# Optimization experiments

Hardware: AMD Instinct MI355X
Metric: run time of the kernel (lower is better)

Reference implementation:

```python
import jax, jax.numpy as jnp
import numpy as np

D = 128
N = 20000
E = 640000
EPS = 1e-5


def setup_inputs() -> dict:
    key = jax.random.key(0)
    ks = jax.random.split(key, 12)
    x = jax.random.normal(ks[0], (N, D), dtype=jnp.float32)
    edge_index = jax.random.randint(ks[1], (2, E), 0, N, dtype=jnp.int64)
    edge_weight = jax.random.uniform(ks[2], (E,), dtype=jnp.float32)
    s = 1.0 / np.sqrt(D)
    # GraphConv params: lin_rel (bias=True) applied to aggregated messages,
    # lin_root (bias=False) applied to root features.
    W_rel = jax.random.uniform(ks[3], (D, D), minval=-s, maxval=s, dtype=jnp.float32)
    b_rel = jax.random.uniform(ks[4], (D,), minval=-s, maxval=s, dtype=jnp.float32)
    W_root = jax.random.uniform(ks[5], (D, D), minval=-s, maxval=s, dtype=jnp.float32)
    # add_linear Linear(out, out)
    lin_W = jax.random.uniform(ks[6], (D, D), minval=-s, maxval=s, dtype=jnp.float32)
    lin_b = jax.random.uniform(ks[7], (D,), minval=-s, maxval=s, dtype=jnp.float32)
    # LayerNorm affine params
    gamma = jnp.ones((D,), dtype=jnp.float32)
    beta = jnp.zeros((D,), dtype=jnp.float32)
    return {"x": x, "edge_index": edge_index, "edge_weight": edge_weight,
            "W_rel": W_rel, "b_rel": b_rel, "W_root": W_root,
            "lin_W": lin_W, "lin_b": lin_b, "gamma": gamma, "beta": beta}


def _layer_norm(h, gamma, beta):
    mu = jnp.mean(h, axis=-1, keepdims=True)
    var = jnp.mean(jnp.square(h - mu), axis=-1, keepdims=True)
    return (h - mu) * jax.lax.rsqrt(var + EPS) * gamma + beta


def reference(x, edge_index, edge_weight, W_rel, b_rel, W_root, lin_W, lin_b, gamma, beta):
    n = x.shape[0]
    src, dst = edge_index[0], edge_index[1]
    # message: edge_weight * x_j, gathered from source nodes
    msg = x[src] * edge_weight[:, None]                      # [E, D]
    # max aggregation to destination nodes; empty segments -> 0 (PyG fill)
    agg = jax.ops.segment_max(msg, dst, num_segments=n)      # [N, D]
    agg = jnp.where(jnp.isneginf(agg), 0.0, agg)
    # GraphConv: lin_rel(agg) + lin_root(x)
    h = agg @ W_rel.T + b_rel + x @ W_root.T                  # [N, D]
    # act + skip + norm
    h = jax.nn.gelu(h, approximate=False) + x
    h = _layer_norm(h, gamma, beta)
    # add_linear branch: act(lin(h)) + skip, then norm (module reuses self.norm)
    h2 = jax.nn.gelu(h @ lin_W.T + lin_b, approximate=False) + h
    h2 = _layer_norm(h2, gamma, beta)
    return h2, edge_weight
```

## Files before the change

### kernel.cpp

```cpp
#include <hip/hip_runtime.h>
#include <math.h>

#define N_NODES 20000
#define N_DIM   128
#define N_EDGES 640000
#define LN_EPS  1e-5f
#define NPW 4
#define CAP 80

#define TASK_E (N_EDGES / 4)
#define TASK_A 160000
#define TASK_B 12288

__device__ __forceinline__ float gelu_exact(float v) {
    return 0.5f * v * (1.0f + erff(v * 0.70710678118654752f));
}
__device__ __forceinline__ float2 fma2(float s, float2 w, float2 a) {
    a.x = fmaf(s, w.x, a.x);
    a.y = fmaf(s, w.y, a.y);
    return a;
}

__device__ __forceinline__ void repack_w(int u, const float* __restrict__ Wr,
                                         const float* __restrict__ Wo,
                                         const float* __restrict__ Wl,
                                         float4* __restrict__ Wp) {
    int m = u >> 12, r2 = u & 4095;
    int kp = r2 >> 6, p = r2 & 63;
    const float* W = (m == 0) ? Wr : ((m == 1) ? Wo : Wl);
    float4 v;
    v.x = W[(2*p)     * N_DIM + 2*kp];
    v.y = W[(2*p + 1) * N_DIM + 2*kp];
    v.z = W[(2*p)     * N_DIM + 2*kp + 1];
    v.w = W[(2*p + 1) * N_DIM + 2*kp + 1];
    Wp[u] = v;
}

__device__ __forceinline__ void node_task(
    int nb, int lane, const char* __restrict__ xb,
    const int* __restrict__ base, const int* __restrict__ dg,
    const int2* __restrict__ eb, const float4* __restrict__ Wp,
    const float* __restrict__ b_rel, const float* __restrict__ lin_b,
    const float* __restrict__ gamma, const float* __restrict__ beta,
    float* __restrict__ out,
    float (*__restrict__ aggw)[N_DIM], float (*__restrict__ xw)[N_DIM])
{
    const int lane8 = lane << 3;

    float2 xsv[NPW];
    #pragma unroll
    for (int r = 0; r < NPW; r++) {
        xsv[r] = *(const float2*)(xb + (size_t)(nb + r) * (N_DIM * 4) + lane8);
        ((float2*)xw[r])[lane] = xsv[r];
    }

    int maxdg = 0;
    #pragma unroll
    for (int r = 0; r < NPW; r++) maxdg = max(maxdg, dg[r]);

    float m0[NPW], m1[NPW];
    #pragma unroll
    for (int r = 0; r < NPW; r++) { m0[r] = -INFINITY; m1[r] = -INFINITY; }

    for (int j = 0; j < maxdg; j += 4) {
        int2 ev[NPW][4];
        #pragma unroll
        for (int r = 0; r < NPW; r++) {
            if (j < dg[r]) {
                int b = base[r] + j, hi = base[r] + dg[r] - 1;
                #pragma unroll
                for (int k = 0; k < 4; k++)
                    ev[r][k] = eb[min(b + k, hi)];
            }
        }
        float2 xv[NPW][4];
        #pragma unroll
        for (int r = 0; r < NPW; r++) {
            if (j < dg[r]) {
                #pragma unroll
                for (int k = 0; k < 4; k++)
                    xv[r][k] = *(const float2*)(xb + (size_t)(unsigned)ev[r][k].x + lane8);
            }
        }
        #pragma unroll
        for (int r = 0; r < NPW; r++) {
            if (j < dg[r]) {
                #pragma unroll
                for (int k = 0; k < 4; k++) {
                    float w = __int_as_float(ev[r][k].y);
                    m0[r] = fmaxf(m0[r], xv[r][k].x * w);
                    m1[r] = fmaxf(m1[r], xv[r][k].y * w);
                }
            }
        }
    }
    #pragma unroll
    for (int r = 0; r < NPW; r++) {
        if (dg[r] == 0) { m0[r] = 0.0f; m1[r] = 0.0f; }
        ((float2*)aggw[r])[lane] = make_float2(m0[r], m1[r]);
    }

    const float4* WpR = Wp;
    const float4* WpO = Wp + 64 * 64;
    const float4* WpL = Wp + 2 * 64 * 64;

    float2 br = ((const float2*)b_rel)[lane];
    float2 acc[NPW];
    #pragma unroll
    for (int r = 0; r < NPW; r++) acc[r] = br;

    for (int i = 0; i < 32; i++) {
        float4 rA = WpR[(2*i)     * 64 + lane];
        float4 rB = WpR[(2*i + 1) * 64 + lane];
        float4 oA = WpO[(2*i)     * 64 + lane];
        float4 oB = WpO[(2*i + 1) * 64 + lane];
        float2 rA01 = make_float2(rA.x, rA.y), rA23 = make_float2(rA.z, rA.w);
        float2 rB01 = make_float2(rB.x, rB.y), rB23 = make_float2(rB.z, rB.w);
        float2 oA01 = make_float2(oA.x, oA.y), oA23 = make_float2(oA.z, oA.w);
        float2 oB01 = make_float2(oB.x, oB.y), oB23 = make_float2(oB.z, oB.w);
        #pragma unroll
        for (int r = 0; r < NPW; r++) {
            float4 a  = *(const float4*)(aggw[r] + 4*i);
            float4 xv = *(const float4*)(xw[r] + 4*i);
            acc[r] = fma2(a.x, rA01, acc[r]);
            acc[r] = fma2(a.y, rA23, acc[r]);
            acc[r] = fma2(a.z, rB01, acc[r]);
            acc[r] = fma2(a.w, rB23, acc[r]);
            acc[r] = fma2(xv.x, oA01, acc[r]);
            acc[r] = fma2(xv.y, oA23, acc[r]);
            acc[r] = fma2(xv.z, oB01, acc[r]);
            acc[r] = fma2(xv.w, oB23, acc[r]);
        }
    }

    float2 gm = ((const float2*)gamma)[lane];
    float2 bt = ((const float2*)beta)[lane];
    float h0[NPW], h1[NPW], s[NPW], v[NPW];
    #pragma unroll
    for (int r = 0; r < NPW; r++) {
        h0[r] = gelu_exact(acc[r].x) + xsv[r].x;
        h1[r] = gelu_exact(acc[r].y) + xsv[r].y;
        s[r] = h0[r] + h1[r];
    }
    #pragma unroll
    for (int m = 32; m; m >>= 1)
        #pragma unroll
        for (int r = 0; r < NPW; r++) s[r] += __shfl_xor(s[r], m);
    #pragma unroll
    for (int r = 0; r < NPW; r++) {
        float mu = s[r] * (1.0f / 128.0f);
        h0[r] -= mu; h1[r] -= mu;
        v[r] = h0[r] * h0[r] + h1[r] * h1[r];
    }
    #pragma unroll
    for (int m = 32; m; m >>= 1)
        #pragma unroll
        for (int r = 0; r < NPW; r++) v[r] += __shfl_xor(v[r], m);
    float2 nrm[NPW];
    #pragma unroll
    for (int r = 0; r < NPW; r++) {
        float rstd = rsqrtf(v[r] * (1.0f / 128.0f) + LN_EPS);
        nrm[r].x = h0[r] * rstd * gm.x + bt.x;
        nrm[r].y = h1[r] * rstd * gm.y + bt.y;
        ((float2*)aggw[r])[lane] = nrm[r];
    }

    float2 lb = ((const float2*)lin_b)[lane];
    float2 acc2[NPW];
    #pragma unroll
    for (int r = 0; r < NPW; r++) acc2[r] = lb;

    for (int i = 0; i < 32; i++) {
        float4 lA = WpL[(2*i)     * 64 + lane];
        float4 lB = WpL[(2*i + 1) * 64 + lane];
        float2 lA01 = make_float2(lA.x, lA.y), lA23 = make_float2(lA.z, lA.w);
        float2 lB01 = make_float2(lB.x, lB.y), lB23 = make_float2(lB.z, lB.w);
        #pragma unroll
        for (int r = 0; r < NPW; r++) {
            float4 h = *(const float4*)(aggw[r] + 4*i);
            acc2[r] = fma2(h.x, lA01, acc2[r]);
            acc2[r] = fma2(h.y, lA23, acc2[r]);
            acc2[r] = fma2(h.z, lB01, acc2[r]);
            acc2[r] = fma2(h.w, lB23, acc2[r]);
        }
    }

    float g0[NPW], g1[NPW];
    #pragma unroll
    for (int r = 0; r < NPW; r++) {
        g0[r] = gelu_exact(acc2[r].x) + nrm[r].x;
        g1[r] = gelu_exact(acc2[r].y) + nrm[r].y;
        s[r] = g0[r] + g1[r];
    }
    #pragma unroll
    for (int m = 32; m; m >>= 1)
        #pragma unroll
        for (int r = 0; r < NPW; r++) s[r] += __shfl_xor(s[r], m);
    #pragma unroll
    for (int r = 0; r < NPW; r++) {
        float mu = s[r] * (1.0f / 128.0f);
        g0[r] -= mu; g1[r] -= mu;
        v[r] = g0[r] * g0[r] + g1[r] * g1[r];
    }
    #pragma unroll
    for (int m = 32; m; m >>= 1)
        #pragma unroll
        for (int r = 0; r < NPW; r++) v[r] += __shfl_xor(v[r], m);
    #pragma unroll
    for (int r = 0; r < NPW; r++) {
        float rstd = rsqrtf(v[r] * (1.0f / 128.0f) + LN_EPS);
        float o0 = g0[r] * rstd * gm.x + bt.x;
        float o1 = g1[r] * rstd * gm.y + bt.y;
        ((float2*)(out + (size_t)(nb + r) * N_DIM))[lane] = make_float2(o0, o1);
    }
}

__global__ __launch_bounds__(256) void edge_pass_kernel(
    const int* __restrict__ ei, const float* __restrict__ ew,
    int* __restrict__ cnt, int2* __restrict__ buck,
    float* __restrict__ out_ew,
    const float* __restrict__ Wr, const float* __restrict__ Wo,
    const float* __restrict__ Wl, float4* __restrict__ Wp)
{
    int t = blockIdx.x * blockDim.x + threadIdx.x;
    if (t < TASK_E) {
        int4 dst = ((const int4*)(ei + N_EDGES))[t];
        int4 src = ((const int4*)ei)[t];
        float4 w = ((const float4*)ew)[t];
        int p0 = atomicAdd(&cnt[dst.x], 1);
        int p1 = atomicAdd(&cnt[dst.y], 1);
        int p2 = atomicAdd(&cnt[dst.z], 1);
        int p3 = atomicAdd(&cnt[dst.w], 1);
        buck[dst.x * CAP + min(p0, CAP - 1)] = make_int2(src.x << 9, __float_as_int(w.x));
        buck[dst.y * CAP + min(p1, CAP - 1)] = make_int2(src.y << 9, __float_as_int(w.y));
        buck[dst.z * CAP + min(p2, CAP - 1)] = make_int2(src.z << 9, __float_as_int(w.z));
        buck[dst.w * CAP + min(p3, CAP - 1)] = make_int2(src.w << 9, __float_as_int(w.w));
    } else if (t < TASK_E + TASK_A) {
        int u = t - TASK_E;
        ((float4*)out_ew)[u] = ((const float4*)ew)[u];
    } else if (t < TASK_E + TASK_A + TASK_B) {
        repack_w(t - TASK_E - TASK_A, Wr, Wo, Wl, Wp);
    }
}

__global__ __launch_bounds__(64) void fused_bucket_kernel(
    const float* __restrict__ x, const int* __restrict__ cnt,
    const int2* __restrict__ buck, const float4* __restrict__ Wp,
    const float* __restrict__ b_rel, const float* __restrict__ lin_b,
    const float* __restrict__ gamma, const float* __restrict__ beta,
    float* __restrict__ out)
{
    __shared__ float agg_s[NPW][N_DIM];
    __shared__ float x_s[NPW][N_DIM];
    const int lane = threadIdx.x & 63;
    const int nb = blockIdx.x * NPW;
    int base[NPW], dg[NPW];
    #pragma unroll
    for (int r = 0; r < NPW; r++) {
        base[r] = (nb + r) * CAP;
        dg[r] = min(__builtin_amdgcn_readfirstlane(cnt[nb + r]), CAP);
    }
    node_task(nb, lane, (const char*)x, base, dg, buck, Wp,
              b_rel, lin_b, gamma, beta, out, agg_s, x_s);
}

__global__ __launch_bounds__(256) void prep_kernel(
    const int* __restrict__ ei, int* __restrict__ deg, int* __restrict__ rank,
    const float* __restrict__ ew, float* __restrict__ out_ew,
    const float* __restrict__ Wr, const float* __restrict__ Wo,
    const float* __restrict__ Wl, float4* __restrict__ Wp)
{
    int t = blockIdx.x * blockDim.x + threadIdx.x;
    if (t < TASK_E) {
        int4 d = ((const int4*)(ei + N_EDGES))[t];
        int4 r;
        r.x = atomicAdd(&deg[d.x], 1);
        r.y = atomicAdd(&deg[d.y], 1);
        r.z = atomicAdd(&deg[d.z], 1);
        r.w = atomicAdd(&deg[d.w], 1);
        ((int4*)rank)[t] = r;
    } else if (t < TASK_E + TASK_A) {
        int u = t - TASK_E;
        ((float4*)out_ew)[u] = ((const float4*)ew)[u];
    } else if (t < TASK_E + TASK_A + TASK_B) {
        repack_w(t - TASK_E - TASK_A, Wr, Wo, Wl, Wp);
    }
}

__global__ __launch_bounds__(1024) void scan_kernel(const int* __restrict__ deg,
                                                    int* __restrict__ off) {
    __shared__ int sm2[1024];
    const int t = threadIdx.x;
    const int lo = t * 20;
    int4 d4[5];
    int s = 0;
    if (lo < N_NODES) {
        #pragma unroll
        for (int i = 0; i < 5; i++) {
            d4[i] = ((const int4*)(deg + lo))[i];
            s += d4[i].x + d4[i].y + d4[i].z + d4[i].w;
        }
    }
    sm2[t] = s;
    __syncthreads();
    for (int d = 1; d < 1024; d <<= 1) {
        int v = (t >= d) ? sm2[t - d] : 0;
        __syncthreads();
        sm2[t] += v;
        __syncthreads();
    }
    int base = sm2[t] - s;
    if (lo < N_NODES) {
        #pragma unroll
        for (int i = 0; i < 5; i++) {
            int4 o;
            o.x = base; base += d4[i].x;
            o.y = base; base += d4[i].y;
            o.z = base; base += d4[i].z;
            o.w = base; base += d4[i].w;
            ((int4*)(off + lo))[i] = o;
        }
    }
    if (t == 1023) off[N_NODES] = base;
}

__global__ __launch_bounds__(256) void fill_kernel(
    const int* __restrict__ ei, const float* __restrict__ ew,
    const int* __restrict__ rank, const int* __restrict__ off,
    int2* __restrict__ csr)
{
    int t = blockIdx.x * blockDim.x + threadIdx.x;
    if (t >= TASK_E) return;
    int4 dst  = ((const int4*)(ei + N_EDGES))[t];
    int4 rk   = ((const int4*)rank)[t];
    int4 src  = ((const int4*)ei)[t];
    float4 w  = ((const float4*)ew)[t];
    csr[off[dst.x] + rk.x] = make_int2(src.x << 9, __float_as_int(w.x));
    csr[off[dst.y] + rk.y] = make_int2(src.y << 9, __float_as_int(w.y));
    csr[off[dst.z] + rk.z] = make_int2(src.z << 9, __float_as_int(w.z));
    csr[off[dst.w] + rk.w] = make_int2(src.w << 9, __float_as_int(w.w));
}

__global__ __launch_bounds__(64) void fused_csr_kernel(
    const float* __restrict__ x, const int* __restrict__ off,
    const int2* __restrict__ csr, const float4* __restrict__ Wp,
    const float* __restrict__ b_rel, const float* __restrict__ lin_b,
    const float* __restrict__ gamma, const float* __restrict__ beta,
    float* __restrict__ out)
{
    __shared__ float agg_s[NPW][N_DIM];
    __shared__ float x_s[NPW][N_DIM];
    const int lane = threadIdx.x & 63;
    const int nb = blockIdx.x * NPW;
    int base[NPW], dg[NPW];
    #pragma unroll
    for (int r = 0; r < NPW; r++) {
        base[r] = __builtin_amdgcn_readfirstlane(off[nb + r]);
        dg[r] = __builtin_amdgcn_readfirstlane(off[nb + r + 1]) - base[r];
    }
    node_task(nb, lane, (const char*)x, base, dg, csr, Wp,
              b_rel, lin_b, gamma, beta, out, agg_s, x_s);
}

extern "C" void kernel_launch(void* const* d_in, const int* in_sizes, int n_in,
                              void* d_out, int out_size, void* d_ws, size_t ws_size,
                              hipStream_t stream) {
    const float* x      = (const float*)d_in[0];
    const int*   ei     = (const int*)  d_in[1];
    const float* ew     = (const float*)d_in[2];
    const float* W_rel  = (const float*)d_in[3];
    const float* b_rel  = (const float*)d_in[4];
    const float* W_root = (const float*)d_in[5];
    const float* lin_W  = (const float*)d_in[6];
    const float* lin_b  = (const float*)d_in[7];
    const float* gamma  = (const float*)d_in[8];
    const float* beta   = (const float*)d_in[9];
    float* out = (float*)d_out;
    float* out_ew = out + (size_t)N_NODES * N_DIM;

    const int n_grid = (TASK_E + TASK_A + TASK_B) / 256;

    const size_t need_bucket = (size_t)N_NODES * 4 + 12288 * 16
                             + (size_t)N_NODES * CAP * 8;
    if (ws_size >= need_bucket) {
        int*    cnt  = (int*)d_ws;
        float4* Wp   = (float4*)((char*)d_ws + (size_t)N_NODES * 4);
        int2*   buck = (int2*)((char*)Wp + 12288 * 16);
        hipMemsetAsync(cnt, 0, N_NODES * sizeof(int), stream);
        edge_pass_kernel<<<n_grid, 256, 0, stream>>>(
            ei, ew, cnt, buck, out_ew, W_rel, W_root, lin_W, Wp);
        fused_bucket_kernel<<<N_NODES / NPW, 64, 0, stream>>>(
            x, cnt, buck, Wp, b_rel, lin_b, gamma, beta, out);
    } else {
        int*    deg  = (int*)d_ws;
        int*    off  = deg + N_NODES;
        int*    rank = off + (N_NODES + 4);
        int2*   csr  = (int2*)(rank + N_EDGES);
        float4* Wp   = (float4*)(csr + N_EDGES);
        hipMemsetAsync(deg, 0, N_NODES * sizeof(int), stream);
        prep_kernel<<<n_grid, 256, 0, stream>>>(
            ei, deg, rank, ew, out_ew, W_rel, W_root, lin_W, Wp);
        scan_kernel<<<1, 1024, 0, stream>>>(deg, off);
        fill_kernel<<<(TASK_E + 255) / 256, 256, 0, stream>>>(ei, ew, rank, off, csr);
        fused_csr_kernel<<<N_NODES / NPW, 64, 0, stream>>>(
            x, off, csr, Wp, b_rel, lin_b, gamma, beta, out);
    }
}
```

Baseline: 193.4 us.

## Gather bf16 copy of node features, process eight nodes per wave, shrink buckets

Adds a bf16 copy of x, built in the edge pass, so the max-aggregation gather reads half the bytes per neighbour. Bucket capacity drops from 80 to 64, and the index shift changes to match the bf16 row stride. NPW goes from 4 to 8 with launch_bounds(64,2), the inner loop processes two edges per step instead of four, and the edge-weight copy is folded into the edge threads. Risks: bf16 rounding of gathered features changes the aggregated values, and nodes with more than 64 in-edges silently overwrite their last bucket slot.

```diff
diff --git a/kernel.cpp b/kernel.cpp
--- a/kernel.cpp
+++ b/kernel.cpp
@@ -5,12 +5,13 @@
 #define N_DIM   128
 #define N_EDGES 640000
 #define LN_EPS  1e-5f
-#define NPW 4
-#define CAP 80
+#define NPW 8
+#define CAP_STD 80
+#define CAP_BF  64
 
 #define TASK_E (N_EDGES / 4)
-#define TASK_A 160000
 #define TASK_B 12288
+#define TASK_X (N_NODES * N_DIM / 8)
 
 __device__ __forceinline__ float gelu_exact(float v) {
     return 0.5f * v * (1.0f + erff(v * 0.70710678118654752f));
@@ -19,6 +20,10 @@
     a.x = fmaf(s, w.x, a.x);
     a.y = fmaf(s, w.y, a.y);
     return a;
+}
+__device__ __forceinline__ unsigned pack_bf16(float f) {
+    unsigned b = __float_as_uint(f);
+    return (b + 0x7FFFu + ((b >> 16) & 1u)) >> 16;
 }
 
 __device__ __forceinline__ void repack_w(int u, const float* __restrict__ Wr,
@@ -36,21 +41,20 @@
     Wp[u] = v;
 }
 
-__device__ __forceinline__ void node_task(
-    int nb, int lane, const char* __restrict__ xb,
-    const int* __restrict__ base, const int* __restrict__ dg,
-    const int2* __restrict__ eb, const float4* __restrict__ Wp,
+template<bool BF16X>
+__device__ __forceinline__ void node_task8(
+    int nb, int lane, const float* __restrict__ x, const char* __restrict__ gxb,
+    const int* base, const int* dg, const int2* __restrict__ eb,
+    const float4* __restrict__ Wp,
     const float* __restrict__ b_rel, const float* __restrict__ lin_b,
     const float* __restrict__ gamma, const float* __restrict__ beta,
     float* __restrict__ out,
     float (*__restrict__ aggw)[N_DIM], float (*__restrict__ xw)[N_DIM])
 {
-    const int lane8 = lane << 3;
-
     float2 xsv[NPW];
     #pragma unroll
     for (int r = 0; r < NPW; r++) {
-        xsv[r] = *(const float2*)(xb + (size_t)(nb + r) * (N_DIM * 4) + lane8);
+        xsv[r] = ((const float2*)(x + (size_t)(nb + r) * N_DIM))[lane];
         ((float2*)xw[r])[lane] = xsv[r];
     }
 
@@ -62,34 +66,52 @@
     #pragma unroll
     for (int r = 0; r < NPW; r++) { m0[r] = -INFINITY; m1[r] = -INFINITY; }
 
-    for (int j = 0; j < maxdg; j += 4) {
-        int2 ev[NPW][4];
+    for (int j = 0; j < maxdg; j += 2) {
+        int2 e0[NPW], e1[NPW];
         #pragma unroll
         for (int r = 0; r < NPW; r++) {
             if (j < dg[r]) {
                 int b = base[r] + j, hi = base[r] + dg[r] - 1;
-                #pragma unroll
-                for (int k = 0; k < 4; k++)
-                    ev[r][k] = eb[min(b + k, hi)];
+                e0[r] = eb[b];
+                e1[r] = eb[min(b + 1, hi)];
             }
         }
-        float2 xv[NPW][4];
-        #pragma unroll
-        for (int r = 0; r < NPW; r++) {
-            if (j < dg[r]) {
-                #pragma unroll
-                for (int k = 0; k < 4; k++)
-                    xv[r][k] = *(const float2*)(xb + (size_t)(unsigned)ev[r][k].x + lane8);
+        if (BF16X) {
+            unsigned u0[NPW], u1[NPW];
+            #pragma unroll
+            for (int r = 0; r < NPW; r++) {
+                if (j < dg[r]) {
+                    u0[r] = *(const unsigned*)(gxb + (size_t)(unsigned)e0[r].x + lane * 4);
+                    u1[r] = *(const unsigned*)(gxb + (size_t)(unsigned)e1[r].x + lane * 4);
+                }
             }
-        }
-        #pragma unroll
-        for (int r = 0; r < NPW; r++) {
-            if (j < dg[r]) {
-                #pragma unroll
-                for (int k = 0; k < 4; k++) {
-                    float w = __int_as_float(ev[r][k].y);
-                    m0[r] = fmaxf(m0[r], xv[r][k].x * w);
-                    m1[r] = fmaxf(m1[r], xv[r][k].y * w);
+            #pragma unroll
+            for (int r = 0; r < NPW; r++) {
+                if (j < dg[r]) {
+                    float w0 = __int_as_float(e0[r].y), w1 = __int_as_float(e1[r].y);
+                    float a0 = __uint_as_float(u0[r] << 16);
+                    float a1 = __uint_as_float(u0[r] & 0xFFFF0000u);
+                    float b0 = __uint_as_float(u1[r] << 16);
+                    float b1 = __uint_as_float(u1[r] & 0xFFFF0000u);
+                    m0[r] = fmaxf(m0[r], fmaxf(a0 * w0, b0 * w1));
+                    m1[r] = fmaxf(m1[r], fmaxf(a1 * w0, b1 * w1));
+                }
+            }
+        } else {
+            float2 v0[NPW], v1[NPW];
+            #pragma unroll
+            for (int r = 0; r < NPW; r++) {
+                if (j < dg[r]) {
+                    v0[r] = *(const float2*)(gxb + (size_t)(unsigned)e0[r].x + lane * 8);
+                    v1[r] = *(const float2*)(gxb + (size_t)(unsigned)e1[r].x + lane * 8);
+                }
+            }
+            #pragma unroll
+            for (int r = 0; r < NPW; r++) {
+                if (j < dg[r]) {
+                    float w0 = __int_as_float(e0[r].y), w1 = __int_as_float(e1[r].y);
+                    m0[r] = fmaxf(m0[r], fmaxf(v0[r].x * w0, v1[r].x * w1));
+                    m1[r] = fmaxf(m1[r], fmaxf(v0[r].y * w0, v1[r].y * w1));
                 }
             }
         }
@@ -215,43 +237,57 @@
     }
 }
 
+template<bool BF16X>
 __global__ __launch_bounds__(256) void edge_pass_kernel(
     const int* __restrict__ ei, const float* __restrict__ ew,
-    int* __restrict__ cnt, int2* __restrict__ buck,
-    float* __restrict__ out_ew,
+    int* __restrict__ cnt, int2* __restrict__ buck, float* __restrict__ out_ew,
     const float* __restrict__ Wr, const float* __restrict__ Wo,
-    const float* __restrict__ Wl, float4* __restrict__ Wp)
-{
+    const float* __restrict__ Wl, float4* __restrict__ Wp,
+    const float* __restrict__ x, unsigned* __restrict__ xbf)
+{
+    const int CAP = BF16X ? CAP_BF : CAP_STD;
+    const int SH  = BF16X ? 8 : 9;
     int t = blockIdx.x * blockDim.x + threadIdx.x;
     if (t < TASK_E) {
         int4 dst = ((const int4*)(ei + N_EDGES))[t];
         int4 src = ((const int4*)ei)[t];
         float4 w = ((const float4*)ew)[t];
+        ((float4*)out_ew)[t] = w;
         int p0 = atomicAdd(&cnt[dst.x], 1);
         int p1 = atomicAdd(&cnt[dst.y], 1);
         int p2 = atomicAdd(&cnt[dst.z], 1);
         int p3 = atomicAdd(&cnt[dst.w], 1);
-        buck[dst.x * CAP + min(p0, CAP - 1)] = make_int2(src.x << 9, __float_as_int(w.x));
-        buck[dst.y * CAP + min(p1, CAP - 1)] = make_int2(src.y << 9, __float_as_int(w.y));
-        buck[dst.z * CAP + min(p2, CAP - 1)] = make_int2(src.z << 9, __float_as_int(w.z));
-        buck[dst.w * CAP + min(p3, CAP - 1)] = make_int2(src.w << 9, __float_as_int(w.w));
-    } else if (t < TASK_E + TASK_A) {
-        int u = t - TASK_E;
-        ((float4*)out_ew)[u] = ((const float4*)ew)[u];
-    } else if (t < TASK_E + TASK_A + TASK_B) {
-        repack_w(t - TASK_E - TASK_A, Wr, Wo, Wl, Wp);
-    }
-}
-
-__global__ __launch_bounds__(64) void fused_bucket_kernel(
-    const float* __restrict__ x, const int* __restrict__ cnt,
-    const int2* __restrict__ buck, const float4* __restrict__ Wp,
+        buck[dst.x * CAP + min(p0, CAP - 1)] = make_int2(src.x << SH, __float_as_int(w.x));
+        buck[dst.y * CAP + min(p1, CAP - 1)] = make_int2(src.y << SH, __float_as_int(w.y));
+        buck[dst.z * CAP + min(p2, CAP - 1)] = make_int2(src.z << SH, __float_as_int(w.z));
+        buck[dst.w * CAP + min(p3, CAP - 1)] = make_int2(src.w << SH, __float_as_int(w.w));
+    } else if (t < TASK_E + TASK_B) {
+        repack_w(t - TASK_E, Wr, Wo, Wl, Wp);
+    } else if (BF16X && t < TASK_E + TASK_B + TASK_X) {
+        int u = t - TASK_E - TASK_B;
+        float4 a = ((const float4*)x)[u * 2];
+        float4 b = ((const float4*)x)[u * 2 + 1];
+        uint4 o;
+        o.x = pack_bf16(a.x) | (pack_bf16(a.y) << 16);
+        o.y = pack_bf16(a.z) | (pack_bf16(a.w) << 16);
+        o.z = pack_bf16(b.x) | (pack_bf16(b.y) << 16);
+        o.w = pack_bf16(b.z) | (pack_bf16(b.w) << 16);
+        ((uint4*)xbf)[u] = o;
+    }
+}
+
+template<bool BF16X>
+__global__ __launch_bounds__(64, 2) void fused_bucket_kernel(
+    const float* __restrict__ x, const char* __restrict__ gxb,
+    const int* __restrict__ cnt, const int2* __restrict__ buck,
+    const float4* __restrict__ Wp,
     const float* __restrict__ b_rel, const float* __restrict__ lin_b,
     const float* __restrict__ gamma, const float* __restrict__ beta,
     float* __restrict__ out)
 {
     __shared__ float agg_s[NPW][N_DIM];
     __shared__ float x_s[NPW][N_DIM];
+    const int CAP = BF16X ? CAP_BF : CAP_STD;
     const int lane = threadIdx.x & 63;
     const int nb = blockIdx.x * NPW;
     int base[NPW], dg[NPW];
@@ -260,8 +296,8 @@
         base[r] = (nb + r) * CAP;
         dg[r] = min(__builtin_amdgcn_readfirstlane(cnt[nb + r]), CAP);
     }
-    node_task(nb, lane, (const char*)x, base, dg, buck, Wp,
-              b_rel, lin_b, gamma, beta, out, agg_s, x_s);
+    node_task8<BF16X>(nb, lane, x, gxb, base, dg, buck, Wp,
+                      b_rel, lin_b, gamma, beta, out, agg_s, x_s);
 }
 
 __global__ __launch_bounds__(256) void prep_kernel(
@@ -273,17 +309,16 @@
     int t = blockIdx.x * blockDim.x + threadIdx.x;
     if (t < TASK_E) {
         int4 d = ((const int4*)(ei + N_EDGES))[t];
+        float4 w = ((const float4*)ew)[t];
+        ((float4*)out_ew)[t] = w;
         int4 r;
         r.x = atomicAdd(&deg[d.x], 1);
         r.y = atomicAdd(&deg[d.y], 1);
         r.z = atomicAdd(&deg[d.z], 1);
         r.w = atomicAdd(&deg[d.w], 1);
         ((int4*)rank)[t] = r;
-    } else if (t < TASK_E + TASK_A) {
-        int u = t - TASK_E;
-        ((float4*)out_ew)[u] = ((const float4*)ew)[u];
-    } else if (t < TASK_E + TASK_A + TASK_B) {
-        repack_w(t - TASK_E - TASK_A, Wr, Wo, Wl, Wp);
+    } else if (t < TASK_E + TASK_B) {
+        repack_w(t - TASK_E, Wr, Wo, Wl, Wp);
     }
 }
 
@@ -341,7 +376,7 @@
     csr[off[dst.w] + rk.w] = make_int2(src.w << 9, __float_as_int(w.w));
 }
 
-__global__ __launch_bounds__(64) void fused_csr_kernel(
+__global__ __launch_bounds__(64, 2) void fused_csr_kernel(
     const float* __restrict__ x, const int* __restrict__ off,
     const int2* __restrict__ csr, const float4* __restrict__ Wp,
     const float* __restrict__ b_rel, const float* __restrict__ lin_b,
@@ -358,8 +393,8 @@
         base[r] = __builtin_amdgcn_readfirstlane(off[nb + r]);
         dg[r] = __builtin_amdgcn_readfirstlane(off[nb + r + 1]) - base[r];
     }
-    node_task(nb, lane, (const char*)x, base, dg, csr, Wp,
-              b_rel, lin_b, gamma, beta, out, agg_s, x_s);
+    node_task8<false>(nb, lane, x, (const char*)x, base, dg, csr, Wp,
+                      b_rel, lin_b, gamma, beta, out, agg_s, x_s);
 }
 
 extern "C" void kernel_launch(void* const* d_in, const int* in_sizes, int n_in,
@@ -378,27 +413,39 @@
     float* out = (float*)d_out;
     float* out_ew = out + (size_t)N_NODES * N_DIM;
 
-    const int n_grid = (TASK_E + TASK_A + TASK_B) / 256;
-
-    const size_t need_bucket = (size_t)N_NODES * 4 + 12288 * 16
-                             + (size_t)N_NODES * CAP * 8;
-    if (ws_size >= need_bucket) {
+    const size_t SZ_CNT = (size_t)N_NODES * 4;
+    const size_t SZ_WP  = (size_t)TASK_B * 16;
+    const size_t SZ_XBF = (size_t)N_NODES * N_DIM * 2;
+    const size_t need_bf  = SZ_CNT + SZ_WP + SZ_XBF + (size_t)N_NODES * CAP_BF * 8;
+    const size_t need_std = SZ_CNT + SZ_WP + (size_t)N_NODES * CAP_STD * 8;
+
+    if (ws_size >= need_bf) {
+        int*      cnt  = (int*)d_ws;
+        float4*   Wp   = (float4*)((char*)d_ws + SZ_CNT);
+        unsigned* xbf  = (unsigned*)((char*)d_ws + SZ_CNT + SZ_WP);
+        int2*     buck = (int2*)((char*)d_ws + SZ_CNT + SZ_WP + SZ_XBF);
+        hipMemsetAsync(cnt, 0, SZ_CNT, stream);
+        edge_pass_kernel<true><<<(TASK_E + TASK_B + TASK_X + 255) / 256, 256, 0, stream>>>(
+            ei, ew, cnt, buck, out_ew, W_rel, W_root, lin_W, Wp, x, xbf);
+        fused_bucket_kernel<true><<<N_NODES / NPW, 64, 0, stream>>>(
+            x, (const char*)xbf, cnt, buck, Wp, b_rel, lin_b, gamma, beta, out);
+    } else if (ws_size >= need_std) {
         int*    cnt  = (int*)d_ws;
-        float4* Wp   = (float4*)((char*)d_ws + (size_t)N_NODES * 4);
-        int2*   buck = (int2*)((char*)Wp + 12288 * 16);
-        hipMemsetAsync(cnt, 0, N_NODES * sizeof(int), stream);
-        edge_pass_kernel<<<n_grid, 256, 0, stream>>>(
-            ei, ew, cnt, buck, out_ew, W_rel, W_root, lin_W, Wp);
-        fused_bucket_kernel<<<N_NODES / NPW, 64, 0, stream>>>(
-            x, cnt, buck, Wp, b_rel, lin_b, gamma, beta, out);
+        float4* Wp   = (float4*)((char*)d_ws + SZ_CNT);
+        int2*   buck = (int2*)((char*)d_ws + SZ_CNT + SZ_WP);
+        hipMemsetAsync(cnt, 0, SZ_CNT, stream);
+        edge_pass_kernel<false><<<(TASK_E + TASK_B + 255) / 256, 256, 0, stream>>>(
+            ei, ew, cnt, buck, out_ew, W_rel, W_root, lin_W, Wp, x, nullptr);
+        fused_bucket_kernel<false><<<N_NODES / NPW, 64, 0, stream>>>(
+            x, (const char*)x, cnt, buck, Wp, b_rel, lin_b, gamma, beta, out);
     } else {
         int*    deg  = (int*)d_ws;
         int*    off  = deg + N_NODES;
         int*    rank = off + (N_NODES + 4);
         int2*   csr  = (int2*)(rank + N_EDGES);
         float4* Wp   = (float4*)(csr + N_EDGES);
-        hipMemsetAsync(deg, 0, N_NODES * sizeof(int), stream);
-        prep_kernel<<<n_grid, 256, 0, stream>>>(
+        hipMemsetAsync(deg, 0, SZ_CNT, stream);
+        prep_kernel<<<(TASK_E + TASK_B + 255) / 256, 256, 0, stream>>>(
             ei, deg, rank, ew, out_ew, W_rel, W_root, lin_W, Wp);
         scan_kernel<<<1, 1024, 0, stream>>>(deg, off);
         fill_kernel<<<(TASK_E + 255) / 256, 256, 0, stream>>>(ei, ew, rank, off, csr);
```

Result: slower. 209.3 us (+8.2%).
